# Performance work log

Hardware: AMD Instinct MI355X
Metric: run time of the kernel (lower is better)

## Reference

```python
import jax, jax.numpy as jnp
import numpy as np

F_BINS, T_STEPS, N_ACTIONS = 257, 65536, 256  # STFT bins, frames, codebook size


def setup_inputs() -> dict:
    key = jax.random.key(0)
    k1, k2, k3, k4 = jax.random.split(key, 4)
    x_out = jax.random.normal(k1, (F_BINS, T_STEPS), dtype=jnp.float32)
    x_source = jax.random.normal(k2, (F_BINS, T_STEPS), dtype=jnp.float32)
    x_clean = jax.random.normal(k3, (F_BINS, T_STEPS), dtype=jnp.float32)
    # G is self.G_mat = G_mat.T, i.e. [freq, action]; gains in [0,1)
    G = jax.random.uniform(k4, (F_BINS, N_ACTIONS), dtype=jnp.float32)
    return {"x_out": x_out, "x_source": x_source, "x_clean": x_clean, "G": G}


def reference(x_out, x_source, x_clean, G):
    # sums[t, a] = sum_f (x_clean[f, t] - G[f, a] * x_source[f, t])
    #            = sum_f x_clean[:, t]  -  (x_source^T @ G)[t, a]
    clean_sum = jnp.sum(x_clean, axis=0)                 # [T]
    proj = jnp.einsum('ft,fa->ta', x_source, G)          # [T, A]
    sums = clean_sum[:, None] - proj                     # [T, A]
    A_t = jnp.argmin(sums, axis=1)                       # [T], values in [0, A)
    F, T = x_source.shape
    # Faithful to the original loop: wiener_true[:, a] = G[:, a] for each
    # SELECTED ACTION a (column indexed by action id, not timestep).
    # Duplicate indices write identical values, so scatter-set is well-defined.
    wiener_true = jnp.zeros((F, T), dtype=x_source.dtype).at[:, A_t].set(G[:, A_t])
    true_out = (wiener_true * x_source).T                # [T, F]
    loss = jnp.mean((true_out - x_out.T) ** 2)
    return loss
```

## Files before the change

### kernel.cpp

```cpp
#include <hip/hip_runtime.h>

#define F_BINS  257
#define T_STEPS 65536
#define N_ACT   256
#define TM      256
#define NBLK_G  256
#define NTHR    512
#define XO_N4   4210688
#define XO_BLKS 2048
#define XO_S    524288

typedef float f32x4 __attribute__((ext_vector_type(4)));
typedef short s16x8 __attribute__((ext_vector_type(8)));
typedef unsigned u32x4 __attribute__((ext_vector_type(4)));
typedef unsigned long long u64;

#define WS_PART  1024
#define WS_CORR  20480
#define WS_MASK  24576
#define WS_GFRAG 65536

__device__ __forceinline__ unsigned short f2bf_rne(float x) {
  unsigned u = __builtin_bit_cast(unsigned, x);
  return (unsigned short)((u + 0x7FFFu + ((u >> 16) & 1u)) >> 16);
}
__device__ __forceinline__ unsigned pack_bf(float hi, float lo) {
  return __builtin_amdgcn_perm(__builtin_bit_cast(unsigned, hi),
                               __builtin_bit_cast(unsigned, lo), 0x07060302u);
}
__device__ __forceinline__ unsigned mono(float v) {
  unsigned u = __builtin_bit_cast(unsigned, v);
  return u ^ (unsigned)(((int)u >> 31) | (int)0x80000000);
}

__global__ __launch_bounds__(256) void k_prep(const float* __restrict__ G,
                                              unsigned char* __restrict__ gfrag) {
  const int u = blockIdx.x * 256 + threadIdx.x;
  const int lane = u & 63, ng = (u >> 6) & 15, kk = u >> 10;
  const int r16 = lane & 15, g = lane >> 4;
  const int a = ng * 16 + r16;
  unsigned short h[8];
#pragma unroll
  for (int j = 0; j < 8; ++j) {
    const int f = kk * 32 + 8 * g + j;
    h[j] = (f < F_BINS) ? f2bf_rne(G[f * N_ACT + a]) : (unsigned short)0;
  }
  u32x4 w;
#pragma unroll
  for (int i = 0; i < 4; ++i)
    w[i] = (unsigned)h[2 * i] | ((unsigned)h[2 * i + 1] << 16);
  *(u32x4*)(gfrag + (size_t)u * 16) = w;
}

__global__ __launch_bounds__(NTHR, 2) void k_gemm(
    const float* __restrict__ xs, const unsigned char* __restrict__ gfrag,
    unsigned* __restrict__ maskp) {
  const int tid = threadIdx.x, lane = tid & 63, wv = tid >> 6;
  const int tq = wv & 3, ah = wv >> 2;
  const int g = lane >> 4, r16 = lane & 15;
  const int t0 = blockIdx.x * TM;
  const int tcol = t0 + 64 * tq + 4 * r16;

  __shared__ __align__(16) unsigned char Bb[147456];
  __shared__ u64 mbuf[2][TM];
  __shared__ unsigned lmask[8];
  if (tid < 8) lmask[tid] = 0u;

#pragma unroll
  for (int i = 0; i < 18; ++i) {
    const int c = 18 * wv + i;
    const unsigned char* src = gfrag + (size_t)c * 1024 + (size_t)lane * 16;
    unsigned char* dst = &Bb[c * 1024];
    __builtin_amdgcn_global_load_lds(
        (const __attribute__((address_space(1))) unsigned*)src,
        (__attribute__((address_space(3))) unsigned*)dst, 16, 0, 0);
  }

#define LOAD_A4(s, kkv)                                                       \
  {                                                                           \
    _Pragma("unroll") for (int j = 0; j < 8; ++j) {                           \
      int f = 32 * (kkv) + 8 * g + j;                                         \
      if ((kkv) == 8) f = f > 256 ? 256 : f;   \
      va[s][j] = *(const float4*)(xs + (size_t)f * T_STEPS + tcol);           \
    }                                                                         \
  }

  float4 va[2][8];
  LOAD_A4(0, 0)
  LOAD_A4(1, 1)
  asm volatile("s_waitcnt vmcnt(16)" ::: "memory");
  __builtin_amdgcn_s_barrier();

  f32x4 acc[4][8];
#pragma unroll
  for (int tau = 0; tau < 4; ++tau)
#pragma unroll
    for (int n = 0; n < 8; ++n) acc[tau][n] = (f32x4){0.f, 0.f, 0.f, 0.f};

#define MKAF(c) __builtin_bit_cast(s16x8, (u32x4){                            \
      pack_bf(va[s][1].c, va[s][0].c), pack_bf(va[s][3].c, va[s][2].c),       \
      pack_bf(va[s][5].c, va[s][4].c), pack_bf(va[s][7].c, va[s][6].c)})

#pragma unroll
  for (int kk = 0; kk < 9; ++kk) {
    const int s = kk & 1;
    s16x8 af[4];
    af[0] = MKAF(x); af[1] = MKAF(y); af[2] = MKAF(z); af[3] = MKAF(w);
    if (kk + 2 <= 8) LOAD_A4(s, kk + 2)
    const unsigned char* bp = &Bb[((kk * 16 + 8 * ah) * 64 + lane) * 16];
#pragma unroll
    for (int n = 0; n < 8; ++n) {
      const s16x8 bfr = *(const s16x8*)(bp + n * 1024);
#pragma unroll
      for (int tau = 0; tau < 4; ++tau)
        acc[tau][n] = __builtin_amdgcn_mfma_f32_16x16x32_bf16(
            af[tau], bfr, acc[tau][n], 0, 0, 0);
    }
  }
#undef LOAD_A4
#undef MKAF

#pragma unroll
  for (int tau = 0; tau < 4; ++tau) {
#pragma unroll
    for (int q = 0; q < 4; ++q) {
      float bv = acc[tau][0][q];
      int   bc = 128 * ah + r16;
#pragma unroll
      for (int n = 1; n < 8; ++n) {
        const int c = 128 * ah + 16 * n + r16;
        if (acc[tau][n][q] > bv) { bv = acc[tau][n][q]; bc = c; }
      }
      u64 key = ((u64)mono(bv) << 32) | (unsigned)(~bc);
#pragma unroll
      for (int m = 1; m <= 8; m <<= 1) {
        const u64 ok = __shfl_xor(key, m, 64);
        if (ok > key) key = ok;
      }
      if (r16 == 0)
        mbuf[ah][64 * tq + 4 * (4 * g + q) + tau] = key;
    }
  }
  __syncthreads();
  if (tid < TM) {
    const u64 k0 = mbuf[0][tid], k1 = mbuf[1][tid];
    const u64 k = k0 >= k1 ? k0 : k1;
    const unsigned bc = ~(unsigned)(k & 0xFFFFFFFFull);
    atomicOr(&lmask[bc >> 5], 1u << (bc & 31));
  }
  __syncthreads();
  if (tid < 8) maskp[blockIdx.x * 8 + tid] = lmask[tid];
}

__global__ __launch_bounds__(256) void k_xo(const float4* __restrict__ xo4,
                                            double* __restrict__ partial) {
  const int tid = threadIdx.x;
  const size_t base = (size_t)blockIdx.x * 256 + tid;
  float4 v[8];
#pragma unroll
  for (int j = 0; j < 8; ++j) v[j] = xo4[base + (size_t)j * XO_S];
  double ds = 0.0;
#pragma unroll
  for (int j = 0; j < 8; ++j)
    ds += (double)fmaf(v[j].x, v[j].x, v[j].y * v[j].y) +
          (double)fmaf(v[j].z, v[j].z, v[j].w * v[j].w);
  if (base < XO_N4 - 8 * XO_S) {
    const float4 w = xo4[8 * XO_S + base];
    ds += (double)fmaf(w.x, w.x, w.y * w.y) + (double)fmaf(w.z, w.z, w.w * w.w);
  }
#pragma unroll
  for (int off = 32; off; off >>= 1) ds += __shfl_down(ds, off);
  __shared__ double sd[4];
  if ((tid & 63) == 0) sd[tid >> 6] = ds;
  __syncthreads();
  if (tid == 0) partial[blockIdx.x] = sd[0] + sd[1] + sd[2] + sd[3];
}

__global__ __launch_bounds__(256) void k_corr(
    const float* __restrict__ xs, const float* __restrict__ xo,
    const float* __restrict__ G, const unsigned* __restrict__ maskp,
    double* __restrict__ corrp) {
  __shared__ unsigned m8[8];
  const int tid = threadIdx.x;
  if (tid < 8) m8[tid] = 0u;
  __syncthreads();
  unsigned m = 0;
  for (int b = tid >> 3; b < NBLK_G; b += 32) m |= maskp[b * 8 + (tid & 7)];
  atomicOr(&m8[tid & 7], m);
  __syncthreads();
  const int f = blockIdx.x, a = tid;
  const bool sel = (m8[a >> 5] >> (a & 31)) & 1u;
  const float gv  = G[f * N_ACT + a];
  const float xsv = xs[(size_t)f * T_STEPS + a];
  const float xov = xo[(size_t)f * T_STEPS + a];
  const float gx  = gv * xsv;
  double acc = sel ? (double)(gx * (gx - 2.f * xov)) : 0.0;
#pragma unroll
  for (int off = 32; off; off >>= 1) acc += __shfl_down(acc, off);
  __shared__ double sdc[4];
  if ((tid & 63) == 0) sdc[tid >> 6] = acc;
  __syncthreads();
  if (tid == 0) corrp[f] = sdc[0] + sdc[1] + sdc[2] + sdc[3];
}

__global__ __launch_bounds__(256) void k_final(const double* __restrict__ partial,
                                               const double* __restrict__ corrp,
                                               float* __restrict__ out) {
  const int tid = threadIdx.x;
  double s = 0.0;
#pragma unroll
  for (int i = 0; i < 8; ++i) s += partial[tid + 256 * i];
  s += corrp[tid];
  if (tid == 0) s += corrp[256];
#pragma unroll
  for (int off = 32; off; off >>= 1) s += __shfl_down(s, off);
  __shared__ double sd[4];
  if ((tid & 63) == 0) sd[tid >> 6] = s;
  __syncthreads();
  if (tid == 0)
    out[0] = (float)((sd[0] + sd[1] + sd[2] + sd[3]) /
                     ((double)F_BINS * (double)T_STEPS));
}

extern "C" void kernel_launch(void* const* d_in, const int* in_sizes, int n_in,
                              void* d_out, int out_size, void* d_ws, size_t ws_size,
                              hipStream_t stream) {
  const float* x_out    = (const float*)d_in[0];
  const float* x_source = (const float*)d_in[1];
  const float* G        = (const float*)d_in[3];

  char* ws = (char*)d_ws;
  double*        partial = (double*)(ws + WS_PART);
  double*        corrp   = (double*)(ws + WS_CORR);
  unsigned*      maskp   = (unsigned*)(ws + WS_MASK);
  unsigned char* gfrag   = (unsigned char*)(ws + WS_GFRAG);

  k_prep <<<36, 256, 0, stream>>>(G, gfrag);
  k_gemm <<<NBLK_G, NTHR, 0, stream>>>(x_source, gfrag, maskp);
  k_xo   <<<XO_BLKS, 256, 0, stream>>>((const float4*)x_out, partial);
  k_corr <<<F_BINS, 256, 0, stream>>>(x_source, x_out, G, maskp, corrp);
  k_final<<<1, 256, 0, stream>>>(partial, corrp, (float*)d_out);
}
```

Measured before the change: 46.15 us.

## Fuse x_out sum-of-squares reduction into the GEMM/argmin kernel

Removes the separate k_xo kernel and has each k_gemm block stream its slice of x_out, accumulating squared values while the MFMA loop runs, plus a small remainder chunk. The aim is to overlap the x_out bandwidth pass with the GEMM and drop one launch and the partials it writes. The cost is more registers and memory traffic inside the GEMM kernel, which only has 256 blocks and may pull less bandwidth than the 2048-block standalone reduction did. Per-thread partials are now summed in fp32 over 16 values before being promoted to double.

```diff
diff --git a/kernel.cpp b/kernel.cpp
--- a/kernel.cpp
+++ b/kernel.cpp
@@ -7,8 +7,8 @@
 #define NBLK_G  256
 #define NTHR    512
 #define XO_N4   4210688
-#define XO_BLKS 2048
-#define XO_S    524288
+#define XO_PB   16384
+#define XO_MAIN (NBLK_G * XO_PB)
 
 typedef float f32x4 __attribute__((ext_vector_type(4)));
 typedef short s16x8 __attribute__((ext_vector_type(8)));
@@ -53,8 +53,9 @@
 }
 
 __global__ __launch_bounds__(NTHR, 2) void k_gemm(
-    const float* __restrict__ xs, const unsigned char* __restrict__ gfrag,
-    unsigned* __restrict__ maskp) {
+    const float* __restrict__ xs, const float4* __restrict__ xo4,
+    const unsigned char* __restrict__ gfrag,
+    unsigned* __restrict__ maskp, double* __restrict__ partial) {
   const int tid = threadIdx.x, lane = tid & 63, wv = tid >> 6;
   const int tq = wv & 3, ah = wv >> 2;
   const int g = lane >> 4, r16 = lane & 15;
@@ -64,6 +65,7 @@
   __shared__ __align__(16) unsigned char Bb[147456];
   __shared__ u64 mbuf[2][TM];
   __shared__ unsigned lmask[8];
+  __shared__ double sdw[8];
   if (tid < 8) lmask[tid] = 0u;
 
 #pragma unroll
@@ -101,12 +103,30 @@
       pack_bf(va[s][1].c, va[s][0].c), pack_bf(va[s][3].c, va[s][2].c),       \
       pack_bf(va[s][5].c, va[s][4].c), pack_bf(va[s][7].c, va[s][6].c)})
 
+  const size_t xbase = (size_t)blockIdx.x * XO_PB + tid;
+  float4 xv[4];
+  double ds = 0.0;
+
 #pragma unroll
   for (int kk = 0; kk < 9; ++kk) {
     const int s = kk & 1;
     s16x8 af[4];
     af[0] = MKAF(x); af[1] = MKAF(y); af[2] = MKAF(z); af[3] = MKAF(w);
     if (kk + 2 <= 8) LOAD_A4(s, kk + 2)
+    if (kk >= 1) {
+      float fs = 0.f;
+#pragma unroll
+      for (int j = 0; j < 4; ++j) {
+        fs = fmaf(xv[j].x, xv[j].x, fs); fs = fmaf(xv[j].y, xv[j].y, fs);
+        fs = fmaf(xv[j].z, xv[j].z, fs); fs = fmaf(xv[j].w, xv[j].w, fs);
+      }
+      ds += (double)fs;
+    }
+    if (kk <= 7) {
+#pragma unroll
+      for (int j = 0; j < 4; ++j)
+        xv[j] = xo4[xbase + (size_t)(kk * 2048 + j * 512)];
+    }
     const unsigned char* bp = &Bb[((kk * 16 + 8 * ah) * 64 + lane) * 16];
 #pragma unroll
     for (int n = 0; n < 8; ++n) {
@@ -119,6 +139,9 @@
   }
 #undef LOAD_A4
 #undef MKAF
+
+  float4 wrem = (float4){0.f, 0.f, 0.f, 0.f};
+  if (tid < 64) wrem = xo4[XO_MAIN + (size_t)blockIdx.x * 64 + tid];
 
 #pragma unroll
   for (int tau = 0; tau < 4; ++tau) {
@@ -150,30 +173,23 @@
   }
   __syncthreads();
   if (tid < 8) maskp[blockIdx.x * 8 + tid] = lmask[tid];
-}
-
-__global__ __launch_bounds__(256) void k_xo(const float4* __restrict__ xo4,
-                                            double* __restrict__ partial) {
-  const int tid = threadIdx.x;
-  const size_t base = (size_t)blockIdx.x * 256 + tid;
-  float4 v[8];
-#pragma unroll
-  for (int j = 0; j < 8; ++j) v[j] = xo4[base + (size_t)j * XO_S];
-  double ds = 0.0;
-#pragma unroll
-  for (int j = 0; j < 8; ++j)
-    ds += (double)fmaf(v[j].x, v[j].x, v[j].y * v[j].y) +
-          (double)fmaf(v[j].z, v[j].z, v[j].w * v[j].w);
-  if (base < XO_N4 - 8 * XO_S) {
-    const float4 w = xo4[8 * XO_S + base];
-    ds += (double)fmaf(w.x, w.x, w.y * w.y) + (double)fmaf(w.z, w.z, w.w * w.w);
+
+  {
+    float fs = 0.f;
+    fs = fmaf(wrem.x, wrem.x, fs); fs = fmaf(wrem.y, wrem.y, fs);
+    fs = fmaf(wrem.z, wrem.z, fs); fs = fmaf(wrem.w, wrem.w, fs);
+    ds += (double)fs;
   }
 #pragma unroll
   for (int off = 32; off; off >>= 1) ds += __shfl_down(ds, off);
-  __shared__ double sd[4];
-  if ((tid & 63) == 0) sd[tid >> 6] = ds;
-  __syncthreads();
-  if (tid == 0) partial[blockIdx.x] = sd[0] + sd[1] + sd[2] + sd[3];
+  if (lane == 0) sdw[wv] = ds;
+  __syncthreads();
+  if (tid == 0) {
+    double s = 0.0;
+#pragma unroll
+    for (int w = 0; w < 8; ++w) s += sdw[w];
+    partial[blockIdx.x] = s;
+  }
 }
 
 __global__ __launch_bounds__(256) void k_corr(
@@ -207,10 +223,7 @@
                                                const double* __restrict__ corrp,
                                                float* __restrict__ out) {
   const int tid = threadIdx.x;
-  double s = 0.0;
-#pragma unroll
-  for (int i = 0; i < 8; ++i) s += partial[tid + 256 * i];
-  s += corrp[tid];
+  double s = partial[tid] + corrp[tid];
   if (tid == 0) s += corrp[256];
 #pragma unroll
   for (int off = 32; off; off >>= 1) s += __shfl_down(s, off);
@@ -236,8 +249,8 @@
   unsigned char* gfrag   = (unsigned char*)(ws + WS_GFRAG);
 
   k_prep <<<36, 256, 0, stream>>>(G, gfrag);
-  k_gemm <<<NBLK_G, NTHR, 0, stream>>>(x_source, gfrag, maskp);
-  k_xo   <<<XO_BLKS, 256, 0, stream>>>((const float4*)x_out, partial);
+  k_gemm <<<NBLK_G, NTHR, 0, stream>>>(x_source, (const float4*)x_out,
+                                       gfrag, maskp, partial);
   k_corr <<<F_BINS, 256, 0, stream>>>(x_source, x_out, G, maskp, corrp);
   k_final<<<1, 256, 0, stream>>>(partial, corrp, (float*)d_out);
 }
```

Result: slower. 49.39 us (+7.0%).

## Fuse G prep with x_out norm reduction and restructure GEMM A-load pipeline

Applied to the files above, without the earlier changes.

The G bf16-fragment prep and the x_out sum-of-squares reduction are merged into one launch, with the reduction reworked to 514 blocks, each doing 32 float4 loads per thread and accumulating in float before converting to double. The GEMM now has each wave own 32 timesteps using float2 loads. All nine A fragments are prefetched and packed before the LDS barrier, and the argmax is done with per-lane shuffles and direct atomicOr instead of an LDS merge buffer. This removes one kernel launch and overlaps x_source loads with the G staging. In exchange it holds more registers for the A fragments, makes narrower global loads, and sums in float precision per thread.

```diff
diff --git a/kernel.cpp b/kernel.cpp
--- a/kernel.cpp
+++ b/kernel.cpp
@@ -7,13 +7,12 @@
 #define NBLK_G  256
 #define NTHR    512
 #define XO_N4   4210688
-#define XO_BLKS 2048
-#define XO_S    524288
+#define XO_BLKS 514
+#define PREP_BLKS 36
 
 typedef float f32x4 __attribute__((ext_vector_type(4)));
 typedef short s16x8 __attribute__((ext_vector_type(8)));
 typedef unsigned u32x4 __attribute__((ext_vector_type(4)));
-typedef unsigned long long u64;
 
 #define WS_PART  1024
 #define WS_CORR  20480
@@ -28,44 +27,77 @@
   return __builtin_amdgcn_perm(__builtin_bit_cast(unsigned, hi),
                                __builtin_bit_cast(unsigned, lo), 0x07060302u);
 }
-__device__ __forceinline__ unsigned mono(float v) {
-  unsigned u = __builtin_bit_cast(unsigned, v);
-  return u ^ (unsigned)(((int)u >> 31) | (int)0x80000000);
-}
-
-__global__ __launch_bounds__(256) void k_prep(const float* __restrict__ G,
-                                              unsigned char* __restrict__ gfrag) {
-  const int u = blockIdx.x * 256 + threadIdx.x;
-  const int lane = u & 63, ng = (u >> 6) & 15, kk = u >> 10;
-  const int r16 = lane & 15, g = lane >> 4;
-  const int a = ng * 16 + r16;
-  unsigned short h[8];
-#pragma unroll
-  for (int j = 0; j < 8; ++j) {
-    const int f = kk * 32 + 8 * g + j;
-    h[j] = (f < F_BINS) ? f2bf_rne(G[f * N_ACT + a]) : (unsigned short)0;
-  }
-  u32x4 w;
-#pragma unroll
-  for (int i = 0; i < 4; ++i)
-    w[i] = (unsigned)h[2 * i] | ((unsigned)h[2 * i + 1] << 16);
-  *(u32x4*)(gfrag + (size_t)u * 16) = w;
+
+__global__ __launch_bounds__(256) void k_pre(
+    const float* __restrict__ G, const float4* __restrict__ xo4,
+    unsigned char* __restrict__ gfrag, double* __restrict__ partial) {
+  const int tid = threadIdx.x;
+  if (blockIdx.x < PREP_BLKS) {
+    const int u = blockIdx.x * 256 + tid;
+    const int lane = u & 63, ng = (u >> 6) & 15, kk = u >> 10;
+    const int r16 = lane & 15, g = lane >> 4;
+    const int a = ng * 16 + r16;
+    unsigned short h[8];
+#pragma unroll
+    for (int j = 0; j < 8; ++j) {
+      const int f = kk * 32 + 8 * g + j;
+      h[j] = (f < F_BINS) ? f2bf_rne(G[f * N_ACT + a]) : (unsigned short)0;
+    }
+    u32x4 w;
+#pragma unroll
+    for (int i = 0; i < 4; ++i)
+      w[i] = (unsigned)h[2 * i] | ((unsigned)h[2 * i + 1] << 16);
+    *(u32x4*)(gfrag + (size_t)u * 16) = w;
+    return;
+  }
+  const int b = blockIdx.x - PREP_BLKS;
+  const size_t base = (size_t)b * 8192 + tid;
+  double ds = 0.0;
+#pragma unroll
+  for (int r = 0; r < 2; ++r) {
+    float4 v[16];
+#pragma unroll
+    for (int j = 0; j < 16; ++j) v[j] = xo4[base + (size_t)(r * 16 + j) * 256];
+    float fs = 0.f;
+#pragma unroll
+    for (int j = 0; j < 16; ++j) {
+      fs = fmaf(v[j].x, v[j].x, fs); fs = fmaf(v[j].y, v[j].y, fs);
+      fs = fmaf(v[j].z, v[j].z, fs); fs = fmaf(v[j].w, v[j].w, fs);
+    }
+    ds += (double)fs;
+  }
+#pragma unroll
+  for (int off = 32; off; off >>= 1) ds += __shfl_down(ds, off);
+  __shared__ double sd[4];
+  if ((tid & 63) == 0) sd[tid >> 6] = ds;
+  __syncthreads();
+  if (tid == 0) partial[b] = sd[0] + sd[1] + sd[2] + sd[3];
 }
 
 __global__ __launch_bounds__(NTHR, 2) void k_gemm(
     const float* __restrict__ xs, const unsigned char* __restrict__ gfrag,
     unsigned* __restrict__ maskp) {
   const int tid = threadIdx.x, lane = tid & 63, wv = tid >> 6;
-  const int tq = wv & 3, ah = wv >> 2;
   const int g = lane >> 4, r16 = lane & 15;
   const int t0 = blockIdx.x * TM;
-  const int tcol = t0 + 64 * tq + 4 * r16;
+  const int tcol = t0 + 32 * wv + 2 * r16;
 
   __shared__ __align__(16) unsigned char Bb[147456];
-  __shared__ u64 mbuf[2][TM];
   __shared__ unsigned lmask[8];
   if (tid < 8) lmask[tid] = 0u;
 
+#define LOADB(slot, kkv)                                                      \
+  {                                                                           \
+    _Pragma("unroll") for (int j = 0; j < 8; ++j) {                           \
+      int f = 32 * (kkv) + 8 * g + j;                                         \
+      if ((kkv) == 8) f = f > 256 ? 256 : f;   \
+      va[slot][j] = *(const float2*)(xs + (size_t)f * T_STEPS + tcol);        \
+    }                                                                         \
+  }
+
+  float2 va[4][8];
+  LOADB(0, 0) LOADB(1, 1) LOADB(2, 2) LOADB(3, 3)
+  __builtin_amdgcn_sched_barrier(0);
 #pragma unroll
   for (int i = 0; i < 18; ++i) {
     const int c = 18 * wv + i;
@@ -75,105 +107,81 @@
         (const __attribute__((address_space(1))) unsigned*)src,
         (__attribute__((address_space(3))) unsigned*)dst, 16, 0, 0);
   }
-
-#define LOAD_A4(s, kkv)                                                       \
-  {                                                                           \
-    _Pragma("unroll") for (int j = 0; j < 8; ++j) {                           \
-      int f = 32 * (kkv) + 8 * g + j;                                         \
-      if ((kkv) == 8) f = f > 256 ? 256 : f;   \
-      va[s][j] = *(const float4*)(xs + (size_t)f * T_STEPS + tcol);           \
-    }                                                                         \
-  }
-
-  float4 va[2][8];
-  LOAD_A4(0, 0)
-  LOAD_A4(1, 1)
-  asm volatile("s_waitcnt vmcnt(16)" ::: "memory");
+  __builtin_amdgcn_sched_barrier(0);
+
+  s16x8 af[9][2];
+#pragma unroll
+  for (int kk = 0; kk < 9; ++kk) {
+    const int b = kk & 3;
+    af[kk][0] = __builtin_bit_cast(s16x8, (u32x4){
+        pack_bf(va[b][1].x, va[b][0].x), pack_bf(va[b][3].x, va[b][2].x),
+        pack_bf(va[b][5].x, va[b][4].x), pack_bf(va[b][7].x, va[b][6].x)});
+    af[kk][1] = __builtin_bit_cast(s16x8, (u32x4){
+        pack_bf(va[b][1].y, va[b][0].y), pack_bf(va[b][3].y, va[b][2].y),
+        pack_bf(va[b][5].y, va[b][4].y), pack_bf(va[b][7].y, va[b][6].y)});
+    if (kk + 4 <= 8) LOADB(b, kk + 4)
+  }
+#undef LOADB
+
+  asm volatile("s_waitcnt vmcnt(0)" ::: "memory");
   __builtin_amdgcn_s_barrier();
 
-  f32x4 acc[4][8];
-#pragma unroll
-  for (int tau = 0; tau < 4; ++tau)
-#pragma unroll
-    for (int n = 0; n < 8; ++n) acc[tau][n] = (f32x4){0.f, 0.f, 0.f, 0.f};
-
-#define MKAF(c) __builtin_bit_cast(s16x8, (u32x4){                            \
-      pack_bf(va[s][1].c, va[s][0].c), pack_bf(va[s][3].c, va[s][2].c),       \
-      pack_bf(va[s][5].c, va[s][4].c), pack_bf(va[s][7].c, va[s][6].c)})
-
-#pragma unroll
-  for (int kk = 0; kk < 9; ++kk) {
-    const int s = kk & 1;
-    s16x8 af[4];
-    af[0] = MKAF(x); af[1] = MKAF(y); af[2] = MKAF(z); af[3] = MKAF(w);
-    if (kk + 2 <= 8) LOAD_A4(s, kk + 2)
-    const unsigned char* bp = &Bb[((kk * 16 + 8 * ah) * 64 + lane) * 16];
+  float bv[2][4]; int bc[2][4];
+#pragma unroll
+  for (int h = 0; h < 2; ++h) {
+    f32x4 acc[2][8];
+#pragma unroll
+    for (int tau = 0; tau < 2; ++tau)
+#pragma unroll
+      for (int n = 0; n < 8; ++n) acc[tau][n] = (f32x4){0.f, 0.f, 0.f, 0.f};
+#pragma unroll
+    for (int kk = 0; kk < 9; ++kk) {
+      const unsigned char* bp = &Bb[((kk * 16 + 8 * h) * 64 + lane) * 16];
+#pragma unroll
+      for (int n = 0; n < 8; ++n) {
+        const s16x8 bfr = *(const s16x8*)(bp + n * 1024);
+        acc[0][n] = __builtin_amdgcn_mfma_f32_16x16x32_bf16(
+            af[kk][0], bfr, acc[0][n], 0, 0, 0);
+        acc[1][n] = __builtin_amdgcn_mfma_f32_16x16x32_bf16(
+            af[kk][1], bfr, acc[1][n], 0, 0, 0);
+      }
+    }
 #pragma unroll
     for (int n = 0; n < 8; ++n) {
-      const s16x8 bfr = *(const s16x8*)(bp + n * 1024);
-#pragma unroll
-      for (int tau = 0; tau < 4; ++tau)
-        acc[tau][n] = __builtin_amdgcn_mfma_f32_16x16x32_bf16(
-            af[tau], bfr, acc[tau][n], 0, 0, 0);
-    }
-  }
-#undef LOAD_A4
-#undef MKAF
-
-#pragma unroll
-  for (int tau = 0; tau < 4; ++tau) {
-#pragma unroll
-    for (int q = 0; q < 4; ++q) {
-      float bv = acc[tau][0][q];
-      int   bc = 128 * ah + r16;
-#pragma unroll
-      for (int n = 1; n < 8; ++n) {
-        const int c = 128 * ah + 16 * n + r16;
-        if (acc[tau][n][q] > bv) { bv = acc[tau][n][q]; bc = c; }
+      const int c = 128 * h + 16 * n + r16;
+#pragma unroll
+      for (int tau = 0; tau < 2; ++tau)
+#pragma unroll
+        for (int q = 0; q < 4; ++q) {
+          const float v = acc[tau][n][q];
+          if (h == 0 && n == 0) { bv[tau][q] = v; bc[tau][q] = c; }
+          else if (v > bv[tau][q]) { bv[tau][q] = v; bc[tau][q] = c; }
+        }
+    }
+  }
+
+#pragma unroll
+  for (int m = 1; m <= 8; m <<= 1) {
+#pragma unroll
+    for (int tau = 0; tau < 2; ++tau)
+#pragma unroll
+      for (int q = 0; q < 4; ++q) {
+        const float ov = __shfl_xor(bv[tau][q], m);
+        const int   oc = __shfl_xor(bc[tau][q], m);
+        if (ov > bv[tau][q] || (ov == bv[tau][q] && oc < bc[tau][q])) {
+          bv[tau][q] = ov; bc[tau][q] = oc;
+        }
       }
-      u64 key = ((u64)mono(bv) << 32) | (unsigned)(~bc);
-#pragma unroll
-      for (int m = 1; m <= 8; m <<= 1) {
-        const u64 ok = __shfl_xor(key, m, 64);
-        if (ok > key) key = ok;
-      }
-      if (r16 == 0)
-        mbuf[ah][64 * tq + 4 * (4 * g + q) + tau] = key;
-    }
-  }
-  __syncthreads();
-  if (tid < TM) {
-    const u64 k0 = mbuf[0][tid], k1 = mbuf[1][tid];
-    const u64 k = k0 >= k1 ? k0 : k1;
-    const unsigned bc = ~(unsigned)(k & 0xFFFFFFFFull);
-    atomicOr(&lmask[bc >> 5], 1u << (bc & 31));
+  }
+  if (r16 == 0) {
+#pragma unroll
+    for (int tau = 0; tau < 2; ++tau)
+#pragma unroll
+      for (int q = 0; q < 4; ++q)
+        atomicOr(&lmask[bc[tau][q] >> 5], 1u << (bc[tau][q] & 31));
   }
   __syncthreads();
   if (tid < 8) maskp[blockIdx.x * 8 + tid] = lmask[tid];
-}
-
-__global__ __launch_bounds__(256) void k_xo(const float4* __restrict__ xo4,
-                                            double* __restrict__ partial) {
-  const int tid = threadIdx.x;
-  const size_t base = (size_t)blockIdx.x * 256 + tid;
-  float4 v[8];
-#pragma unroll
-  for (int j = 0; j < 8; ++j) v[j] = xo4[base + (size_t)j * XO_S];
-  double ds = 0.0;
-#pragma unroll
-  for (int j = 0; j < 8; ++j)
-    ds += (double)fmaf(v[j].x, v[j].x, v[j].y * v[j].y) +
-          (double)fmaf(v[j].z, v[j].z, v[j].w * v[j].w);
-  if (base < XO_N4 - 8 * XO_S) {
-    const float4 w = xo4[8 * XO_S + base];
-    ds += (double)fmaf(w.x, w.x, w.y * w.y) + (double)fmaf(w.z, w.z, w.w * w.w);
-  }
-#pragma unroll
-  for (int off = 32; off; off >>= 1) ds += __shfl_down(ds, off);
-  __shared__ double sd[4];
-  if ((tid & 63) == 0) sd[tid >> 6] = ds;
-  __syncthreads();
-  if (tid == 0) partial[blockIdx.x] = sd[0] + sd[1] + sd[2] + sd[3];
 }
 
 __global__ __launch_bounds__(256) void k_corr(
@@ -207,10 +215,8 @@
                                                const double* __restrict__ corrp,
                                                float* __restrict__ out) {
   const int tid = threadIdx.x;
-  double s = 0.0;
-#pragma unroll
-  for (int i = 0; i < 8; ++i) s += partial[tid + 256 * i];
-  s += corrp[tid];
+  double s = partial[tid] + partial[tid + 256] + corrp[tid];
+  if (tid < 2) s += partial[tid + 512];
   if (tid == 0) s += corrp[256];
 #pragma unroll
   for (int off = 32; off; off >>= 1) s += __shfl_down(s, off);
@@ -235,9 +241,9 @@
   unsigned*      maskp   = (unsigned*)(ws + WS_MASK);
   unsigned char* gfrag   = (unsigned char*)(ws + WS_GFRAG);
 
-  k_prep <<<36, 256, 0, stream>>>(G, gfrag);
+  k_pre  <<<PREP_BLKS + XO_BLKS, 256, 0, stream>>>(G, (const float4*)x_out,
+                                                   gfrag, partial);
   k_gemm <<<NBLK_G, NTHR, 0, stream>>>(x_source, gfrag, maskp);
-  k_xo   <<<XO_BLKS, 256, 0, stream>>>((const float4*)x_out, partial);
   k_corr <<<F_BINS, 256, 0, stream>>>(x_source, x_out, G, maskp, corrp);
   k_final<<<1, 256, 0, stream>>>(partial, corrp, (float*)d_out);
 }
```

Result: faster. 44.68 us (-3.2%).
